# Kernel tuning notes

Measured on AMD Instinct MI355X. Metric: run time of the kernel, lower is better.

## Reference

```python
import jax, jax.numpy as jnp
import numpy as np

V, NJ, NSHAPE, NEXP, B = 5023, 5, 100, 50, 1024
PARENTS = np.array([-1, 0, 1, 1, 1])  # FLAME kinematic tree: global, neck, jaw, eyeL, eyeR


def rodrigues(rot_vecs):
    """Axis-angle [..., 3] -> rotation matrices [..., 3, 3] (SMPL-style, eps-safe)."""
    angle = jnp.linalg.norm(rot_vecs + 1e-8, axis=-1, keepdims=True)  # [...,1]
    axis = rot_vecs / angle
    cos = jnp.cos(angle)[..., None]
    sin = jnp.sin(angle)[..., None]
    rx, ry, rz = axis[..., 0], axis[..., 1], axis[..., 2]
    z = jnp.zeros_like(rx)
    K = jnp.stack([z, -rz, ry, rz, z, -rx, -ry, rx, z], axis=-1).reshape(rot_vecs.shape[:-1] + (3, 3))
    eye = jnp.eye(3, dtype=rot_vecs.dtype)
    return eye + sin * K + (1.0 - cos) * (K @ K)


def setup_inputs() -> dict:
    ks = jax.random.split(jax.random.key(0), 8)
    shape_params = jax.random.normal(ks[0], (B, NSHAPE), jnp.float32)
    expression_params = jax.random.normal(ks[1], (B, NEXP), jnp.float32)
    pose_params = 0.1 * jax.random.normal(ks[2], (B, 6), jnp.float32)
    v_template = jax.random.normal(ks[3], (V, 3), jnp.float32)
    shapedirs = 0.01 * jax.random.normal(ks[4], (V, 3, NSHAPE + NEXP), jnp.float32)
    posedirs = 0.01 * jax.random.normal(ks[5], ((NJ - 1) * 9, V * 3), jnp.float32)
    jr = jax.random.uniform(ks[6], (NJ, V), jnp.float32)
    J_regressor = jr / jr.sum(axis=1, keepdims=True)
    w = jax.random.uniform(ks[7], (V, NJ), jnp.float32)
    lbs_weights = w / w.sum(axis=1, keepdims=True)
    return dict(shape_params=shape_params, expression_params=expression_params,
                pose_params=pose_params, v_template=v_template, shapedirs=shapedirs,
                posedirs=posedirs, J_regressor=J_regressor, lbs_weights=lbs_weights)


def reference(shape_params, expression_params, pose_params, v_template,
              shapedirs, posedirs, J_regressor, lbs_weights):
    b = shape_params.shape[0]
    dt = shape_params.dtype
    # full_pose = [global(3), neck(3)=0, jaw(3), eyes(6)=0]
    zeros3 = jnp.zeros((b, 3), dt)
    zeros6 = jnp.zeros((b, 6), dt)
    full_pose = jnp.concatenate([pose_params[:, :3], zeros3, pose_params[:, 3:], zeros6], axis=1)
    betas = jnp.concatenate([shape_params, expression_params], axis=1)  # [b, 150]

    # shape blendshapes
    v_shaped = v_template[None] + jnp.einsum('bl,vcl->bvc', betas, shapedirs)  # [b,V,3]
    joints = jnp.einsum('jv,bvc->bjc', J_regressor, v_shaped)                 # [b,J,3]

    # pose blendshapes
    rot_mats = rodrigues(full_pose.reshape(b, NJ, 3))                         # [b,J,3,3]
    eye3 = jnp.eye(3, dtype=dt)
    pose_feature = (rot_mats[:, 1:] - eye3).reshape(b, (NJ - 1) * 9)
    v_posed = v_shaped + (pose_feature @ posedirs).reshape(b, V, 3)

    # rigid kinematic chain
    rel_joints = joints.at[:, 1:].add(-joints[:, PARENTS[1:]])                # [b,J,3]
    bottom = jnp.broadcast_to(jnp.array([0.0, 0.0, 0.0, 1.0], dt), (b, NJ, 1, 4))
    tmats = jnp.concatenate([jnp.concatenate([rot_mats, rel_joints[..., None]], axis=-1), bottom], axis=-2)  # [b,J,4,4]
    chain = [tmats[:, 0]]
    for i in range(1, NJ):  # fixed 5-joint tree
        chain.append(chain[PARENTS[i]] @ tmats[:, i])
    transforms = jnp.stack(chain, axis=1)                                     # [b,J,4,4]
    joints_h = jnp.concatenate([joints, jnp.zeros((b, NJ, 1), dt)], axis=-1)[..., None]  # [b,J,4,1]
    rel_transforms = transforms - jnp.pad(transforms @ joints_h, ((0, 0), (0, 0), (0, 0), (3, 0)))  # [b,J,4,4]

    # linear blend skinning
    T = jnp.einsum('vj,bjxy->bvxy', lbs_weights, rel_transforms)              # [b,V,4,4]
    v_h = jnp.concatenate([v_posed, jnp.ones((b, V, 1), dt)], axis=-1)        # [b,V,4]
    vertices = jnp.einsum('bvxy,bvy->bvx', T, v_h)[..., :3]                   # [b,V,3]
    return vertices, T
```

## Files before the change

### kernel.cpp

```cpp
#include <hip/hip_runtime.h>

#define VN     5023
#define NBETA  150
#define NBP    152
#define NL4    38
#define VP     5024
#define NBATCH 1024
#define N3     15069
#define BT     16

__global__ void k0_t4(const float* __restrict__ sd, const float* __restrict__ vt,
                      float4* __restrict__ sdpT4) {
    int i = blockIdx.x * 256 + threadIdx.x;
    if (i >= 3 * NL4 * VP) return;
    int c   = i / (NL4 * VP);
    int rem = i - c * (NL4 * VP);
    int l4  = rem / VP;
    int v   = rem - l4 * VP;
    float4 out = make_float4(0.f, 0.f, 0.f, 0.f);
    if (v < VN) {
        int row = v * 3 + c;
        float vals[4];
#pragma unroll
        for (int q = 0; q < 4; q++) {
            int ll = l4 * 4 + q;
            vals[q] = (ll < NBETA) ? sd[row * NBETA + ll]
                     : ((ll == NBETA) ? vt[row] : 0.f);
        }
        out = make_float4(vals[0], vals[1], vals[2], vals[3]);
    }
    sdpT4[i] = out;
}

__global__ void k1_t4(const float* __restrict__ jr, const float4* __restrict__ sdpT4,
                      float* __restrict__ JS) {
    int j3c = blockIdx.x, l4 = blockIdx.y;
    int j = j3c / 3, c = j3c - 3 * j;
    int t = threadIdx.x;
    const float4* col = sdpT4 + (size_t)(c * NL4 + l4) * VP;
    float4 acc = make_float4(0.f, 0.f, 0.f, 0.f);
    for (int v = t; v < VN; v += 256) {
        float w = jr[j * VN + v];
        float4 s = col[v];
        acc.x += w * s.x; acc.y += w * s.y; acc.z += w * s.z; acc.w += w * s.w;
    }
    __shared__ float4 red[256];
    red[t] = acc; __syncthreads();
    for (int s = 128; s > 0; s >>= 1) {
        if (t < s) {
            red[t].x += red[t + s].x; red[t].y += red[t + s].y;
            red[t].z += red[t + s].z; red[t].w += red[t + s].w;
        }
        __syncthreads();
    }
    if (t == 0) {
        JS[j3c * NBP + l4 * 4 + 0] = red[0].x;
        JS[j3c * NBP + l4 * 4 + 1] = red[0].y;
        JS[j3c * NBP + l4 * 4 + 2] = red[0].z;
        JS[j3c * NBP + l4 * 4 + 3] = red[0].w;
    }
}

__device__ __forceinline__ void rodrigues3(float x, float y, float z, float* R) {
    float ax = x + 1e-8f, ay = y + 1e-8f, az = z + 1e-8f;
    float ang = sqrtf(ax * ax + ay * ay + az * az);
    float inv = 1.0f / ang;
    float ux = x * inv, uy = y * inv, uz = z * inv;
    float co = cosf(ang), si = sinf(ang), t1 = 1.0f - co;
    float K[9] = {0.f, -uz, uy,  uz, 0.f, -ux,  -uy, ux, 0.f};
    float K2[9];
#pragma unroll
    for (int r = 0; r < 3; r++)
#pragma unroll
        for (int cc = 0; cc < 3; cc++) {
            float a = 0.f;
#pragma unroll
            for (int k = 0; k < 3; k++) a += K[r * 3 + k] * K[k * 3 + cc];
            K2[r * 3 + cc] = a;
        }
#pragma unroll
    for (int i = 0; i < 9; i++) {
        float e = (i == 0 || i == 4 || i == 8) ? 1.f : 0.f;
        R[i] = e + si * K[i] + t1 * K2[i];
    }
}

__global__ void k2_pose(const float* __restrict__ shp, const float* __restrict__ expr,
                        const float* __restrict__ pose, const float* __restrict__ JS,
                        float* __restrict__ betasF, float* __restrict__ pf9,
                        float* __restrict__ rel) {
    int b = blockIdx.x;
    int tt = threadIdx.x;
    __shared__ float sB[NBP];
    __shared__ float sJ[15];
    for (int l = tt; l < NBP; l += 64) {
        float val = 0.0f;
        if (l < 100) val = shp[b * 100 + l];
        else if (l < 150) val = expr[b * 50 + (l - 100)];
        else if (l == 150) val = 1.0f;
        sB[l] = val;
        betasF[b * NBP + l] = val;
    }
    __syncthreads();
    if (tt < 15) {
        float acc = 0.0f;
        const float* row = JS + tt * NBP;
        for (int l = 0; l < NBP; ++l) acc += row[l] * sB[l];
        sJ[tt] = acc;
    }
    __syncthreads();
    if (tt == 0) {
        float p[6];
#pragma unroll
        for (int i = 0; i < 6; i++) p[i] = pose[b * 6 + i];
        float R0[9], RJ[9];
        rodrigues3(p[0], p[1], p[2], R0);
        rodrigues3(p[3], p[4], p[5], RJ);
        float Jm[5][3];
#pragma unroll
        for (int jj = 0; jj < 5; jj++)
#pragma unroll
            for (int cc = 0; cc < 3; cc++) Jm[jj][cc] = sJ[jj * 3 + cc];
        float rj[5][3];
#pragma unroll
        for (int cc = 0; cc < 3; cc++) {
            rj[0][cc] = Jm[0][cc];
            rj[1][cc] = Jm[1][cc] - Jm[0][cc];
            rj[2][cc] = Jm[2][cc] - Jm[1][cc];
            rj[3][cc] = Jm[3][cc] - Jm[1][cc];
            rj[4][cc] = Jm[4][cc] - Jm[1][cc];
        }
        float tw[5][3];
#pragma unroll
        for (int cc = 0; cc < 3; cc++) tw[0][cc] = rj[0][cc];
#pragma unroll
        for (int cc = 0; cc < 3; cc++)
            tw[1][cc] = R0[cc * 3 + 0] * rj[1][0] + R0[cc * 3 + 1] * rj[1][1] + R0[cc * 3 + 2] * rj[1][2] + tw[0][cc];
#pragma unroll
        for (int jj = 2; jj < 5; jj++)
#pragma unroll
            for (int cc = 0; cc < 3; cc++)
                tw[jj][cc] = R0[cc * 3 + 0] * rj[jj][0] + R0[cc * 3 + 1] * rj[jj][1] + R0[cc * 3 + 2] * rj[jj][2] + tw[1][cc];
        float R2w[9];
#pragma unroll
        for (int r = 0; r < 3; r++)
#pragma unroll
            for (int cc = 0; cc < 3; cc++) {
                float a = 0.f;
#pragma unroll
                for (int k = 0; k < 3; k++) a += R0[r * 3 + k] * RJ[k * 3 + cc];
                R2w[r * 3 + cc] = a;
            }
        float* ro = rel + b * 80;
#pragma unroll
        for (int jj = 0; jj < 5; jj++) {
            const float* Rw = (jj == 2) ? R2w : R0;
#pragma unroll
            for (int rr = 0; rr < 3; rr++) {
                ro[jj * 16 + rr * 4 + 0] = Rw[rr * 3 + 0];
                ro[jj * 16 + rr * 4 + 1] = Rw[rr * 3 + 1];
                ro[jj * 16 + rr * 4 + 2] = Rw[rr * 3 + 2];
                float tj = Rw[rr * 3 + 0] * Jm[jj][0] + Rw[rr * 3 + 1] * Jm[jj][1] + Rw[rr * 3 + 2] * Jm[jj][2];
                ro[jj * 16 + rr * 4 + 3] = tw[jj][rr] - tj;
            }
            ro[jj * 16 + 12] = 0.f; ro[jj * 16 + 13] = 0.f; ro[jj * 16 + 14] = 0.f; ro[jj * 16 + 15] = 1.f;
        }
        float* pf = pf9 + b * 12;
#pragma unroll
        for (int e = 0; e < 9; e++) pf[e] = RJ[e] - ((e == 0 || e == 4 || e == 8) ? 1.f : 0.f);
        pf[9] = 0.f; pf[10] = 0.f; pf[11] = 0.f;
    }
}

__global__ void __launch_bounds__(128, 2)
k3_main(const float4* __restrict__ sdpT4, const float* __restrict__ pd,
        const float* __restrict__ lw,
        const float* __restrict__ betasF, const float* __restrict__ pf9,
        const float* __restrict__ rel,
        float* __restrict__ outv, float* __restrict__ outT) {
    int tid = threadIdx.x;
    int v = blockIdx.x * 128 + tid;
    bool ok = v < VN;
    int vc = ok ? v : VN - 1;
    int b0 = blockIdx.y * BT;

    float acc[3][BT];
#pragma unroll
    for (int c = 0; c < 3; c++)
#pragma unroll
        for (int bb = 0; bb < BT; bb++) acc[c][bb] = 0.0f;

    const float4* sp = sdpT4 + vc;

#pragma unroll 1
    for (int l0 = 0; l0 < NBP; l0 += 8) {
        int i0 = l0 >> 2;
        const float4 a0  = sp[(size_t)(0 * NL4 + i0) * VP];
        const float4 a1  = sp[(size_t)(0 * NL4 + i0 + 1) * VP];
        const float4 b0q = sp[(size_t)(1 * NL4 + i0) * VP];
        const float4 b1q = sp[(size_t)(1 * NL4 + i0 + 1) * VP];
        const float4 c0q = sp[(size_t)(2 * NL4 + i0) * VP];
        const float4 c1q = sp[(size_t)(2 * NL4 + i0 + 1) * VP];
        float s0[8] = {a0.x, a0.y, a0.z, a0.w, a1.x, a1.y, a1.z, a1.w};
        float s1[8] = {b0q.x, b0q.y, b0q.z, b0q.w, b1q.x, b1q.y, b1q.z, b1q.w};
        float s2[8] = {c0q.x, c0q.y, c0q.z, c0q.w, c1q.x, c1q.y, c1q.z, c1q.w};
#pragma unroll
        for (int bb = 0; bb < BT; bb++) {
            const float* brow = betasF + (size_t)(b0 + bb) * NBP + l0;
            const float4 be0 = *(const float4*)(brow);
            const float4 be1 = *(const float4*)(brow + 4);
            float be[8] = {be0.x, be0.y, be0.z, be0.w, be1.x, be1.y, be1.z, be1.w};
#pragma unroll
            for (int k = 0; k < 8; k++) {
                acc[0][bb] += be[k] * s0[k];
                acc[1][bb] += be[k] * s1[k];
                acc[2][bb] += be[k] * s2[k];
            }
        }
    }

    if (!ok) return;

    float wj[5], pdv[9][3];
#pragma unroll
    for (int j = 0; j < 5; j++) wj[j] = lw[v * 5 + j];
#pragma unroll
    for (int k = 0; k < 9; k++)
#pragma unroll
        for (int c = 0; c < 3; c++) pdv[k][c] = pd[(size_t)(9 + k) * N3 + v * 3 + c];

#pragma unroll
    for (int bb = 0; bb < BT; bb++) {
        int b = b0 + bb;
        const float* pf = pf9 + b * 12;
        const float* rb = rel + b * 80;
        float vp[3];
#pragma unroll
        for (int c = 0; c < 3; c++) {
            float x = acc[c][bb];
#pragma unroll
            for (int k = 0; k < 9; k++) x += pf[k] * pdv[k][c];
            vp[c] = x;
        }
        float T[16];
#pragma unroll
        for (int e = 0; e < 16; e++) T[e] = 0.0f;
#pragma unroll
        for (int j = 0; j < 5; j++) {
            float w = wj[j];
            const float4 r0 = *(const float4*)(rb + j * 16 + 0);
            const float4 r1 = *(const float4*)(rb + j * 16 + 4);
            const float4 r2 = *(const float4*)(rb + j * 16 + 8);
            const float4 r3 = *(const float4*)(rb + j * 16 + 12);
            T[0]  += w * r0.x;  T[1]  += w * r0.y;  T[2]  += w * r0.z;  T[3]  += w * r0.w;
            T[4]  += w * r1.x;  T[5]  += w * r1.y;  T[6]  += w * r1.z;  T[7]  += w * r1.w;
            T[8]  += w * r2.x;  T[9]  += w * r2.y;  T[10] += w * r2.z;  T[11] += w * r2.w;
            T[12] += w * r3.x;  T[13] += w * r3.y;  T[14] += w * r3.z;  T[15] += w * r3.w;
        }
        float vo[3];
#pragma unroll
        for (int rr = 0; rr < 3; rr++)
            vo[rr] = T[rr * 4 + 0] * vp[0] + T[rr * 4 + 1] * vp[1] + T[rr * 4 + 2] * vp[2] + T[rr * 4 + 3];

        size_t vbase = (size_t)b * VN + v;
        float* pv = outv + vbase * 3;
        pv[0] = vo[0];
        pv[1] = vo[1];
        pv[2] = vo[2];
        float4* pT = (float4*)(outT + vbase * 16);
        pT[0] = make_float4(T[0],  T[1],  T[2],  T[3]);
        pT[1] = make_float4(T[4],  T[5],  T[6],  T[7]);
        pT[2] = make_float4(T[8],  T[9],  T[10], T[11]);
        pT[3] = make_float4(T[12], T[13], T[14], T[15]);
    }
}

extern "C" void kernel_launch(void* const* d_in, const int* in_sizes, int n_in,
                              void* d_out, int out_size, void* d_ws, size_t ws_size,
                              hipStream_t stream) {
    const float* shp  = (const float*)d_in[0];
    const float* expr = (const float*)d_in[1];
    const float* pose = (const float*)d_in[2];
    const float* vt   = (const float*)d_in[3];
    const float* sd   = (const float*)d_in[4];
    const float* pd   = (const float*)d_in[5];
    const float* jr   = (const float*)d_in[6];
    const float* lw   = (const float*)d_in[7];

    float* outv = (float*)d_out;
    float* outT = outv + (size_t)NBATCH * VN * 3;

    char* w = (char*)d_ws;
    const size_t SDPT_B  = (size_t)3 * NL4 * VP * 16;
    const size_t JS_B    = 15 * NBP * 4;
    const size_t BETAS_B = (size_t)NBATCH * NBP * 4;
    const size_t PF9_B   = (size_t)NBATCH * 12 * 4;
    float4* sdpT4 = (float4*)w;
    float* JS     = (float*)(w + SDPT_B);
    float* betasF = (float*)(w + SDPT_B + JS_B);
    float* pf9    = (float*)(w + SDPT_B + JS_B + BETAS_B);
    float* rel    = (float*)(w + SDPT_B + JS_B + BETAS_B + PF9_B);

    k0_t4<<<(3 * NL4 * VP + 255) / 256, 256, 0, stream>>>(sd, vt, sdpT4);
    k1_t4<<<dim3(15, NL4), 256, 0, stream>>>(jr, sdpT4, JS);
    k2_pose<<<NBATCH, 64, 0, stream>>>(shp, expr, pose, JS, betasF, pf9, rel);
    k3_main<<<dim3(40, NBATCH / BT), 128, 0, stream>>>(sdpT4, pd, lw, betasF, pf9, rel, outv, outT);
}
```

Baseline: 238.9 us.

## Process two vertices per thread with prefetched shapedir loads in main kernel

The main kernel changes its register tile from 1 vertex × 16 batches to 2 vertices × 8 batches per thread, so each loaded beta value is reused across two vertices. It also software-prefetches the next iteration's shapedir float4 loads into registers before the current FMAs. The grid halves in x and doubles in y, keeping the total work the same. The cost is higher register pressure, and each shapedir element is now read by twice as many batch blocks.

```diff
diff --git a/kernel.cpp b/kernel.cpp
--- a/kernel.cpp
+++ b/kernel.cpp
@@ -7,7 +7,8 @@
 #define VP     5024
 #define NBATCH 1024
 #define N3     15069
-#define BT     16
+#define BT     8
+#define VPT    2
 
 __global__ void k0_t4(const float* __restrict__ sd, const float* __restrict__ vt,
                       float4* __restrict__ sdpT4) {
@@ -179,31 +180,47 @@
         const float* __restrict__ rel,
         float* __restrict__ outv, float* __restrict__ outT) {
     int tid = threadIdx.x;
-    int v = blockIdx.x * 128 + tid;
-    bool ok = v < VN;
-    int vc = ok ? v : VN - 1;
+    int vA = blockIdx.x * 256 + tid;
+    int vB = vA + 128;
+    bool okA = vA < VN, okB = vB < VN;
+    int vcA = okA ? vA : VN - 1;
+    int vcB = okB ? vB : VN - 1;
     int b0 = blockIdx.y * BT;
 
-    float acc[3][BT];
+    float accA[3][BT], accB[3][BT];
 #pragma unroll
     for (int c = 0; c < 3; c++)
 #pragma unroll
-        for (int bb = 0; bb < BT; bb++) acc[c][bb] = 0.0f;
-
-    const float4* sp = sdpT4 + vc;
+        for (int bb = 0; bb < BT; bb++) { accA[c][bb] = 0.0f; accB[c][bb] = 0.0f; }
+
+    const float4* spA = sdpT4 + vcA;
+    const float4* spB = sdpT4 + vcB;
+
+    float4 nA0 = spA[(size_t)(0 * NL4) * VP],     nA1 = spA[(size_t)(0 * NL4 + 1) * VP];
+    float4 nB0 = spA[(size_t)(1 * NL4) * VP],     nB1 = spA[(size_t)(1 * NL4 + 1) * VP];
+    float4 nC0 = spA[(size_t)(2 * NL4) * VP],     nC1 = spA[(size_t)(2 * NL4 + 1) * VP];
+    float4 mA0 = spB[(size_t)(0 * NL4) * VP],     mA1 = spB[(size_t)(0 * NL4 + 1) * VP];
+    float4 mB0 = spB[(size_t)(1 * NL4) * VP],     mB1 = spB[(size_t)(1 * NL4 + 1) * VP];
+    float4 mC0 = spB[(size_t)(2 * NL4) * VP],     mC1 = spB[(size_t)(2 * NL4 + 1) * VP];
 
 #pragma unroll 1
     for (int l0 = 0; l0 < NBP; l0 += 8) {
-        int i0 = l0 >> 2;
-        const float4 a0  = sp[(size_t)(0 * NL4 + i0) * VP];
-        const float4 a1  = sp[(size_t)(0 * NL4 + i0 + 1) * VP];
-        const float4 b0q = sp[(size_t)(1 * NL4 + i0) * VP];
-        const float4 b1q = sp[(size_t)(1 * NL4 + i0 + 1) * VP];
-        const float4 c0q = sp[(size_t)(2 * NL4 + i0) * VP];
-        const float4 c1q = sp[(size_t)(2 * NL4 + i0 + 1) * VP];
-        float s0[8] = {a0.x, a0.y, a0.z, a0.w, a1.x, a1.y, a1.z, a1.w};
-        float s1[8] = {b0q.x, b0q.y, b0q.z, b0q.w, b1q.x, b1q.y, b1q.z, b1q.w};
-        float s2[8] = {c0q.x, c0q.y, c0q.z, c0q.w, c1q.x, c1q.y, c1q.z, c1q.w};
+        float4 a0 = nA0, a1 = nA1, b0q = nB0, b1q = nB1, c0q = nC0, c1q = nC1;
+        float4 d0 = mA0, d1 = mA1, e0q = mB0, e1q = mB1, f0q = mC0, f1q = mC1;
+        int i0n = (l0 + 8 < NBP) ? ((l0 + 8) >> 2) : 0;
+        nA0 = spA[(size_t)(0 * NL4 + i0n) * VP];  nA1 = spA[(size_t)(0 * NL4 + i0n + 1) * VP];
+        nB0 = spA[(size_t)(1 * NL4 + i0n) * VP];  nB1 = spA[(size_t)(1 * NL4 + i0n + 1) * VP];
+        nC0 = spA[(size_t)(2 * NL4 + i0n) * VP];  nC1 = spA[(size_t)(2 * NL4 + i0n + 1) * VP];
+        mA0 = spB[(size_t)(0 * NL4 + i0n) * VP];  mA1 = spB[(size_t)(0 * NL4 + i0n + 1) * VP];
+        mB0 = spB[(size_t)(1 * NL4 + i0n) * VP];  mB1 = spB[(size_t)(1 * NL4 + i0n + 1) * VP];
+        mC0 = spB[(size_t)(2 * NL4 + i0n) * VP];  mC1 = spB[(size_t)(2 * NL4 + i0n + 1) * VP];
+
+        float sA0[8] = {a0.x, a0.y, a0.z, a0.w, a1.x, a1.y, a1.z, a1.w};
+        float sA1[8] = {b0q.x, b0q.y, b0q.z, b0q.w, b1q.x, b1q.y, b1q.z, b1q.w};
+        float sA2[8] = {c0q.x, c0q.y, c0q.z, c0q.w, c1q.x, c1q.y, c1q.z, c1q.w};
+        float sB0[8] = {d0.x, d0.y, d0.z, d0.w, d1.x, d1.y, d1.z, d1.w};
+        float sB1[8] = {e0q.x, e0q.y, e0q.z, e0q.w, e1q.x, e1q.y, e1q.z, e1q.w};
+        float sB2[8] = {f0q.x, f0q.y, f0q.z, f0q.w, f1q.x, f1q.y, f1q.z, f1q.w};
 #pragma unroll
         for (int bb = 0; bb < BT; bb++) {
             const float* brow = betasF + (size_t)(b0 + bb) * NBP + l0;
@@ -212,66 +229,73 @@
             float be[8] = {be0.x, be0.y, be0.z, be0.w, be1.x, be1.y, be1.z, be1.w};
 #pragma unroll
             for (int k = 0; k < 8; k++) {
-                acc[0][bb] += be[k] * s0[k];
-                acc[1][bb] += be[k] * s1[k];
-                acc[2][bb] += be[k] * s2[k];
-            }
-        }
-    }
-
-    if (!ok) return;
-
-    float wj[5], pdv[9][3];
-#pragma unroll
-    for (int j = 0; j < 5; j++) wj[j] = lw[v * 5 + j];
-#pragma unroll
-    for (int k = 0; k < 9; k++)
-#pragma unroll
-        for (int c = 0; c < 3; c++) pdv[k][c] = pd[(size_t)(9 + k) * N3 + v * 3 + c];
-
-#pragma unroll
-    for (int bb = 0; bb < BT; bb++) {
-        int b = b0 + bb;
-        const float* pf = pf9 + b * 12;
-        const float* rb = rel + b * 80;
-        float vp[3];
-#pragma unroll
-        for (int c = 0; c < 3; c++) {
-            float x = acc[c][bb];
-#pragma unroll
-            for (int k = 0; k < 9; k++) x += pf[k] * pdv[k][c];
-            vp[c] = x;
-        }
-        float T[16];
-#pragma unroll
-        for (int e = 0; e < 16; e++) T[e] = 0.0f;
-#pragma unroll
-        for (int j = 0; j < 5; j++) {
-            float w = wj[j];
-            const float4 r0 = *(const float4*)(rb + j * 16 + 0);
-            const float4 r1 = *(const float4*)(rb + j * 16 + 4);
-            const float4 r2 = *(const float4*)(rb + j * 16 + 8);
-            const float4 r3 = *(const float4*)(rb + j * 16 + 12);
-            T[0]  += w * r0.x;  T[1]  += w * r0.y;  T[2]  += w * r0.z;  T[3]  += w * r0.w;
-            T[4]  += w * r1.x;  T[5]  += w * r1.y;  T[6]  += w * r1.z;  T[7]  += w * r1.w;
-            T[8]  += w * r2.x;  T[9]  += w * r2.y;  T[10] += w * r2.z;  T[11] += w * r2.w;
-            T[12] += w * r3.x;  T[13] += w * r3.y;  T[14] += w * r3.z;  T[15] += w * r3.w;
-        }
-        float vo[3];
-#pragma unroll
-        for (int rr = 0; rr < 3; rr++)
-            vo[rr] = T[rr * 4 + 0] * vp[0] + T[rr * 4 + 1] * vp[1] + T[rr * 4 + 2] * vp[2] + T[rr * 4 + 3];
-
-        size_t vbase = (size_t)b * VN + v;
-        float* pv = outv + vbase * 3;
-        pv[0] = vo[0];
-        pv[1] = vo[1];
-        pv[2] = vo[2];
-        float4* pT = (float4*)(outT + vbase * 16);
-        pT[0] = make_float4(T[0],  T[1],  T[2],  T[3]);
-        pT[1] = make_float4(T[4],  T[5],  T[6],  T[7]);
-        pT[2] = make_float4(T[8],  T[9],  T[10], T[11]);
-        pT[3] = make_float4(T[12], T[13], T[14], T[15]);
+                accA[0][bb] += be[k] * sA0[k];
+                accA[1][bb] += be[k] * sA1[k];
+                accA[2][bb] += be[k] * sA2[k];
+                accB[0][bb] += be[k] * sB0[k];
+                accB[1][bb] += be[k] * sB1[k];
+                accB[2][bb] += be[k] * sB2[k];
+            }
+        }
+    }
+
+#pragma unroll
+    for (int half = 0; half < VPT; half++) {
+        int v = (half == 0) ? vA : vB;
+        bool ok = (half == 0) ? okA : okB;
+        if (!ok) continue;
+        float wj[5], pdv[9][3];
+#pragma unroll
+        for (int j = 0; j < 5; j++) wj[j] = lw[v * 5 + j];
+#pragma unroll
+        for (int k = 0; k < 9; k++)
+#pragma unroll
+            for (int c = 0; c < 3; c++) pdv[k][c] = pd[(size_t)(9 + k) * N3 + v * 3 + c];
+
+#pragma unroll
+        for (int bb = 0; bb < BT; bb++) {
+            int b = b0 + bb;
+            const float* pf = pf9 + b * 12;
+            const float* rb = rel + b * 80;
+            float vp[3];
+#pragma unroll
+            for (int c = 0; c < 3; c++) {
+                float x = (half == 0) ? accA[c][bb] : accB[c][bb];
+#pragma unroll
+                for (int k = 0; k < 9; k++) x += pf[k] * pdv[k][c];
+                vp[c] = x;
+            }
+            float T[16];
+#pragma unroll
+            for (int e = 0; e < 16; e++) T[e] = 0.0f;
+#pragma unroll
+            for (int j = 0; j < 5; j++) {
+                float w = wj[j];
+                const float4 r0 = *(const float4*)(rb + j * 16 + 0);
+                const float4 r1 = *(const float4*)(rb + j * 16 + 4);
+                const float4 r2 = *(const float4*)(rb + j * 16 + 8);
+                const float4 r3 = *(const float4*)(rb + j * 16 + 12);
+                T[0]  += w * r0.x;  T[1]  += w * r0.y;  T[2]  += w * r0.z;  T[3]  += w * r0.w;
+                T[4]  += w * r1.x;  T[5]  += w * r1.y;  T[6]  += w * r1.z;  T[7]  += w * r1.w;
+                T[8]  += w * r2.x;  T[9]  += w * r2.y;  T[10] += w * r2.z;  T[11] += w * r2.w;
+                T[12] += w * r3.x;  T[13] += w * r3.y;  T[14] += w * r3.z;  T[15] += w * r3.w;
+            }
+            float vo[3];
+#pragma unroll
+            for (int rr = 0; rr < 3; rr++)
+                vo[rr] = T[rr * 4 + 0] * vp[0] + T[rr * 4 + 1] * vp[1] + T[rr * 4 + 2] * vp[2] + T[rr * 4 + 3];
+
+            size_t vbase = (size_t)b * VN + v;
+            float* pv = outv + vbase * 3;
+            pv[0] = vo[0];
+            pv[1] = vo[1];
+            pv[2] = vo[2];
+            float4* pT = (float4*)(outT + vbase * 16);
+            pT[0] = make_float4(T[0],  T[1],  T[2],  T[3]);
+            pT[1] = make_float4(T[4],  T[5],  T[6],  T[7]);
+            pT[2] = make_float4(T[8],  T[9],  T[10], T[11]);
+            pT[3] = make_float4(T[12], T[13], T[14], T[15]);
+        }
     }
 }
 
@@ -304,5 +328,5 @@
     k0_t4<<<(3 * NL4 * VP + 255) / 256, 256, 0, stream>>>(sd, vt, sdpT4);
     k1_t4<<<dim3(15, NL4), 256, 0, stream>>>(jr, sdpT4, JS);
     k2_pose<<<NBATCH, 64, 0, stream>>>(shp, expr, pose, JS, betasF, pf9, rel);
-    k3_main<<<dim3(40, NBATCH / BT), 128, 0, stream>>>(sdpT4, pd, lw, betasF, pf9, rel, outv, outT);
-}
+    k3_main<<<dim3((VN + 255) / 256, NBATCH / BT), 128, 0, stream>>>(sdpT4, pd, lw, betasF, pf9, rel, outv, outT);
+}
```

New measurement: 329.0 us. +37.7%, slower.

## Split batch tile into two chunks with register-prefetched shapedir loads

Applied to the files above, without the earlier changes.

The 16-batch tile is processed as two 8-batch chunks. Each chunk runs its own blend-shape GEMV loop, with the next iteration's shapedir float4 loads prefetched into registers, and then runs the skinning epilogue and stores. This lowers accumulator register pressure and interleaves the heavy output stores with compute, but it reads the shapedir stream twice per block and adds live prefetch registers.

```diff
diff --git a/kernel.cpp b/kernel.cpp
--- a/kernel.cpp
+++ b/kernel.cpp
@@ -8,6 +8,7 @@
 #define NBATCH 1024
 #define N3     15069
 #define BT     16
+#define BC     8
 
 __global__ void k0_t4(const float* __restrict__ sd, const float* __restrict__ vt,
                       float4* __restrict__ sdpT4) {
@@ -172,6 +173,59 @@
     }
 }
 
+__device__ __forceinline__ void epilogue8(const float acc[3][BC], int b0c, int v,
+                                          const float* __restrict__ wj,
+                                          const float pdv[9][3],
+                                          const float* __restrict__ pf9,
+                                          const float* __restrict__ rel,
+                                          float* __restrict__ outv,
+                                          float* __restrict__ outT) {
+#pragma unroll
+    for (int bb = 0; bb < BC; bb++) {
+        int b = b0c + bb;
+        const float* pf = pf9 + b * 12;
+        const float* rb = rel + b * 80;
+        float vp[3];
+#pragma unroll
+        for (int c = 0; c < 3; c++) {
+            float x = acc[c][bb];
+#pragma unroll
+            for (int k = 0; k < 9; k++) x += pf[k] * pdv[k][c];
+            vp[c] = x;
+        }
+        float T[16];
+#pragma unroll
+        for (int e = 0; e < 16; e++) T[e] = 0.0f;
+#pragma unroll
+        for (int j = 0; j < 5; j++) {
+            float w = wj[j];
+            const float4 r0 = *(const float4*)(rb + j * 16 + 0);
+            const float4 r1 = *(const float4*)(rb + j * 16 + 4);
+            const float4 r2 = *(const float4*)(rb + j * 16 + 8);
+            const float4 r3 = *(const float4*)(rb + j * 16 + 12);
+            T[0]  += w * r0.x;  T[1]  += w * r0.y;  T[2]  += w * r0.z;  T[3]  += w * r0.w;
+            T[4]  += w * r1.x;  T[5]  += w * r1.y;  T[6]  += w * r1.z;  T[7]  += w * r1.w;
+            T[8]  += w * r2.x;  T[9]  += w * r2.y;  T[10] += w * r2.z;  T[11] += w * r2.w;
+            T[12] += w * r3.x;  T[13] += w * r3.y;  T[14] += w * r3.z;  T[15] += w * r3.w;
+        }
+        float vo[3];
+#pragma unroll
+        for (int rr = 0; rr < 3; rr++)
+            vo[rr] = T[rr * 4 + 0] * vp[0] + T[rr * 4 + 1] * vp[1] + T[rr * 4 + 2] * vp[2] + T[rr * 4 + 3];
+
+        size_t vbase = (size_t)b * VN + v;
+        float* pv = outv + vbase * 3;
+        pv[0] = vo[0];
+        pv[1] = vo[1];
+        pv[2] = vo[2];
+        float4* pT = (float4*)(outT + vbase * 16);
+        pT[0] = make_float4(T[0],  T[1],  T[2],  T[3]);
+        pT[1] = make_float4(T[4],  T[5],  T[6],  T[7]);
+        pT[2] = make_float4(T[8],  T[9],  T[10], T[11]);
+        pT[3] = make_float4(T[12], T[13], T[14], T[15]);
+    }
+}
+
 __global__ void __launch_bounds__(128, 2)
 k3_main(const float4* __restrict__ sdpT4, const float* __restrict__ pd,
         const float* __restrict__ lw,
@@ -184,94 +238,62 @@
     int vc = ok ? v : VN - 1;
     int b0 = blockIdx.y * BT;
 
-    float acc[3][BT];
-#pragma unroll
-    for (int c = 0; c < 3; c++)
-#pragma unroll
-        for (int bb = 0; bb < BT; bb++) acc[c][bb] = 0.0f;
-
     const float4* sp = sdpT4 + vc;
 
+    float wj[5], pdv[9][3];
+    bool epiLoaded = false;
+
+#pragma unroll
+    for (int chunk = 0; chunk < 2; chunk++) {
+        int b0c = b0 + chunk * BC;
+        float acc[3][BC];
+#pragma unroll
+        for (int c = 0; c < 3; c++)
+#pragma unroll
+            for (int bb = 0; bb < BC; bb++) acc[c][bb] = 0.0f;
+
+        float4 nA0 = sp[(size_t)(0 * NL4) * VP],  nA1 = sp[(size_t)(0 * NL4 + 1) * VP];
+        float4 nB0 = sp[(size_t)(1 * NL4) * VP],  nB1 = sp[(size_t)(1 * NL4 + 1) * VP];
+        float4 nC0 = sp[(size_t)(2 * NL4) * VP],  nC1 = sp[(size_t)(2 * NL4 + 1) * VP];
+
 #pragma unroll 1
-    for (int l0 = 0; l0 < NBP; l0 += 8) {
-        int i0 = l0 >> 2;
-        const float4 a0  = sp[(size_t)(0 * NL4 + i0) * VP];
-        const float4 a1  = sp[(size_t)(0 * NL4 + i0 + 1) * VP];
-        const float4 b0q = sp[(size_t)(1 * NL4 + i0) * VP];
-        const float4 b1q = sp[(size_t)(1 * NL4 + i0 + 1) * VP];
-        const float4 c0q = sp[(size_t)(2 * NL4 + i0) * VP];
-        const float4 c1q = sp[(size_t)(2 * NL4 + i0 + 1) * VP];
-        float s0[8] = {a0.x, a0.y, a0.z, a0.w, a1.x, a1.y, a1.z, a1.w};
-        float s1[8] = {b0q.x, b0q.y, b0q.z, b0q.w, b1q.x, b1q.y, b1q.z, b1q.w};
-        float s2[8] = {c0q.x, c0q.y, c0q.z, c0q.w, c1q.x, c1q.y, c1q.z, c1q.w};
-#pragma unroll
-        for (int bb = 0; bb < BT; bb++) {
-            const float* brow = betasF + (size_t)(b0 + bb) * NBP + l0;
-            const float4 be0 = *(const float4*)(brow);
-            const float4 be1 = *(const float4*)(brow + 4);
-            float be[8] = {be0.x, be0.y, be0.z, be0.w, be1.x, be1.y, be1.z, be1.w};
-#pragma unroll
-            for (int k = 0; k < 8; k++) {
-                acc[0][bb] += be[k] * s0[k];
-                acc[1][bb] += be[k] * s1[k];
-                acc[2][bb] += be[k] * s2[k];
+        for (int l0 = 0; l0 < NBP; l0 += 8) {
+            float4 a0 = nA0, a1 = nA1, b0q = nB0, b1q = nB1, c0q = nC0, c1q = nC1;
+            int i0n = (l0 + 8 < NBP) ? ((l0 + 8) >> 2) : 0;
+            nA0 = sp[(size_t)(0 * NL4 + i0n) * VP];  nA1 = sp[(size_t)(0 * NL4 + i0n + 1) * VP];
+            nB0 = sp[(size_t)(1 * NL4 + i0n) * VP];  nB1 = sp[(size_t)(1 * NL4 + i0n + 1) * VP];
+            nC0 = sp[(size_t)(2 * NL4 + i0n) * VP];  nC1 = sp[(size_t)(2 * NL4 + i0n + 1) * VP];
+
+            float s0[8] = {a0.x, a0.y, a0.z, a0.w, a1.x, a1.y, a1.z, a1.w};
+            float s1[8] = {b0q.x, b0q.y, b0q.z, b0q.w, b1q.x, b1q.y, b1q.z, b1q.w};
+            float s2[8] = {c0q.x, c0q.y, c0q.z, c0q.w, c1q.x, c1q.y, c1q.z, c1q.w};
+#pragma unroll
+            for (int bb = 0; bb < BC; bb++) {
+                const float* brow = betasF + (size_t)(b0c + bb) * NBP + l0;
+                const float4 be0 = *(const float4*)(brow);
+                const float4 be1 = *(const float4*)(brow + 4);
+                float be[8] = {be0.x, be0.y, be0.z, be0.w, be1.x, be1.y, be1.z, be1.w};
+#pragma unroll
+                for (int k = 0; k < 8; k++) {
+                    acc[0][bb] += be[k] * s0[k];
+                    acc[1][bb] += be[k] * s1[k];
+                    acc[2][bb] += be[k] * s2[k];
+                }
             }
         }
-    }
-
-    if (!ok) return;
-
-    float wj[5], pdv[9][3];
-#pragma unroll
-    for (int j = 0; j < 5; j++) wj[j] = lw[v * 5 + j];
-#pragma unroll
-    for (int k = 0; k < 9; k++)
-#pragma unroll
-        for (int c = 0; c < 3; c++) pdv[k][c] = pd[(size_t)(9 + k) * N3 + v * 3 + c];
-
-#pragma unroll
-    for (int bb = 0; bb < BT; bb++) {
-        int b = b0 + bb;
-        const float* pf = pf9 + b * 12;
-        const float* rb = rel + b * 80;
-        float vp[3];
-#pragma unroll
-        for (int c = 0; c < 3; c++) {
-            float x = acc[c][bb];
-#pragma unroll
-            for (int k = 0; k < 9; k++) x += pf[k] * pdv[k][c];
-            vp[c] = x;
-        }
-        float T[16];
-#pragma unroll
-        for (int e = 0; e < 16; e++) T[e] = 0.0f;
-#pragma unroll
-        for (int j = 0; j < 5; j++) {
-            float w = wj[j];
-            const float4 r0 = *(const float4*)(rb + j * 16 + 0);
-            const float4 r1 = *(const float4*)(rb + j * 16 + 4);
-            const float4 r2 = *(const float4*)(rb + j * 16 + 8);
-            const float4 r3 = *(const float4*)(rb + j * 16 + 12);
-            T[0]  += w * r0.x;  T[1]  += w * r0.y;  T[2]  += w * r0.z;  T[3]  += w * r0.w;
-            T[4]  += w * r1.x;  T[5]  += w * r1.y;  T[6]  += w * r1.z;  T[7]  += w * r1.w;
-            T[8]  += w * r2.x;  T[9]  += w * r2.y;  T[10] += w * r2.z;  T[11] += w * r2.w;
-            T[12] += w * r3.x;  T[13] += w * r3.y;  T[14] += w * r3.z;  T[15] += w * r3.w;
-        }
-        float vo[3];
-#pragma unroll
-        for (int rr = 0; rr < 3; rr++)
-            vo[rr] = T[rr * 4 + 0] * vp[0] + T[rr * 4 + 1] * vp[1] + T[rr * 4 + 2] * vp[2] + T[rr * 4 + 3];
-
-        size_t vbase = (size_t)b * VN + v;
-        float* pv = outv + vbase * 3;
-        pv[0] = vo[0];
-        pv[1] = vo[1];
-        pv[2] = vo[2];
-        float4* pT = (float4*)(outT + vbase * 16);
-        pT[0] = make_float4(T[0],  T[1],  T[2],  T[3]);
-        pT[1] = make_float4(T[4],  T[5],  T[6],  T[7]);
-        pT[2] = make_float4(T[8],  T[9],  T[10], T[11]);
-        pT[3] = make_float4(T[12], T[13], T[14], T[15]);
+
+        if (ok) {
+            if (!epiLoaded) {
+                epiLoaded = true;
+#pragma unroll
+                for (int j = 0; j < 5; j++) wj[j] = lw[v * 5 + j];
+#pragma unroll
+                for (int k = 0; k < 9; k++)
+#pragma unroll
+                    for (int c = 0; c < 3; c++) pdv[k][c] = pd[(size_t)(9 + k) * N3 + v * 3 + c];
+            }
+            epilogue8(acc, b0c, v, wj, pdv, pf9, rel, outv, outT);
+        }
     }
 }
 
```

After: 331.0 us. 38.5% more time.
